# Optimization experiments

Measured on AMD Instinct MI355X. Metric: run time of the kernel, lower is better.

## Reference

```python
import jax, jax.numpy as jnp
import numpy as np

T = 96
CAP_MWH = 800.0
DP_RAMP = 65.0
DT = 0.25
ETA = float(np.sqrt(0.91))
L_MIN = 4
MAX_CHARGE_MWH = 1200.0
P_MAX = 195.0
N = 5 * T  # variable layout: [c, d, yc, yd, soc]
ITERS = 400  # fixed PDHG iterations (stand-in for SCS to eps=1e-5)

_VOFF = {'c': 0, 'd': 1, 'yc': 2, 'yd': 3, 'soc': 4}

def _idx(v, t):
    return _VOFF[v] * T + t

def _build_lp():
    G, h, A, b = [], [], [], []
    def ineq(pairs, rhs):
        r = np.zeros(N)
        for v, t, co in pairs:
            r[_idx(v, t)] += co
        G.append(r); h.append(rhs)
    def eq(pairs, rhs):
        r = np.zeros(N)
        for v, t, co in pairs:
            r[_idx(v, t)] += co
        A.append(r); b.append(rhs)
    for t in range(T):
        ineq([('c', t, 1.0)], P_MAX); ineq([('d', t, 1.0)], P_MAX)
        ineq([('c', t, -1.0)], 0.0); ineq([('d', t, -1.0)], 0.0)
        ineq([('yc', t, -1.0)], 0.0); ineq([('yc', t, 1.0)], 1.0)
        ineq([('yd', t, -1.0)], 0.0); ineq([('yd', t, 1.0)], 1.0)
        ineq([('soc', t, -1.0)], 0.0); ineq([('soc', t, 1.0)], CAP_MWH)
        ineq([('yc', t, 1.0), ('yd', t, 1.0)], 1.0)
        ineq([('c', t, 1.0), ('yc', t, -P_MAX)], 0.0)
        ineq([('d', t, 1.0), ('yd', t, -P_MAX)], 0.0)
    for t in range(1, T):
        ineq([('c', t, 1.0), ('c', t - 1, -1.0)], DP_RAMP)
        ineq([('c', t - 1, 1.0), ('c', t, -1.0)], DP_RAMP)
        ineq([('d', t, 1.0), ('d', t - 1, -1.0)], DP_RAMP)
        ineq([('d', t - 1, 1.0), ('d', t, -1.0)], DP_RAMP)
    for t in range(T - 1):
        ineq([('yc', t, 1.0), ('yd', t + 1, 1.0)], 1.0)
        ineq([('yd', t, 1.0), ('yc', t + 1, 1.0)], 1.0)
    for v in ('yc', 'yd'):
        for t in range(T):
            for k in range(1, L_MIN):
                if t + k >= T:
                    break
                if t > 0:
                    ineq([(v, t + k, -1.0), (v, t, 1.0), (v, t - 1, -1.0)], 0.0)
                else:
                    ineq([(v, t + k, -1.0), (v, t, 1.0)], 0.0)
    ineq([('c', t, DT) for t in range(T)], MAX_CHARGE_MWH)
    eq([('soc', 0, 1.0), ('c', 0, -ETA * DT), ('d', 0, DT / ETA)], 0.0)
    for t in range(1, T):
        eq([('soc', t, 1.0), ('soc', t - 1, -1.0), ('c', t, -ETA * DT), ('d', t, DT / ETA)], 0.0)
    eq([('soc', T - 1, 1.0)], 0.0)
    return np.array(G), np.array(h), np.array(A), np.array(b)

_G, _h, _A, _b = _build_lp()
_M_EQ = _A.shape[0]
_K_np = np.vstack([_A, _G]).astype(np.float32)
_kb_np = np.concatenate([_b, _h]).astype(np.float32)
_LNORM = float(np.linalg.norm(_K_np.astype(np.float64), 2))
TAU = np.float32(0.9 / _LNORM)
SIG = np.float32(0.9 / _LNORM)
K_MAT = jnp.asarray(_K_np)     # (M, N)
KB = jnp.asarray(_kb_np)       # (M,)


def _solve_one(price):
    # LP: min q^T x  s.t.  A x = b, G x <= h   (max price.(d-c)*DT)
    q = DT * jnp.concatenate([price, -price, jnp.zeros(3 * T, price.dtype)])
    def step(carry, _):
        x, y = carry
        x_new = x - TAU * (q + K_MAT.T @ y)
        x_bar = 2.0 * x_new - x
        y_new = y + SIG * (K_MAT @ x_bar - KB)
        # dual cone projection: equality duals free, inequality duals >= 0
        y_new = jnp.concatenate([y_new[:_M_EQ], jnp.maximum(y_new[_M_EQ:], 0.0)])
        return (x_new, y_new), None
    x0 = jnp.zeros(N, price.dtype)
    y0 = jnp.zeros(K_MAT.shape[0], price.dtype)
    (x, _), _ = jax.lax.scan(step, (x0, y0), None, length=ITERS)
    return x[:T], x[T:2 * T]  # (c, d)


def setup_inputs() -> dict:
    key = jax.random.key(0)
    # realistic-ish electricity prices: ~N(400, 100) CNY/MWh
    price = 400.0 + 100.0 * jax.random.normal(key, (256, T), dtype=jnp.float32)
    return {"price_pred": price}


def reference(price_pred):
    c, d = jax.vmap(_solve_one)(price_pred)  # each (B, 96)
    return c, d
```

## Files before the change

### kernel.cpp

```cpp
#include <hip/hip_runtime.h>
#include <math.h>


#define NITER 400
#define PITER 10
#define NY 1874
#define NX 520

__device__ __forceinline__ float wave_sum64(float v) {
  float r = v;
  int x;
  x = __builtin_amdgcn_update_dpp(0, __float_as_int(r), 0x111, 0xf, 0xf, true);
  r += __int_as_float(x);
  x = __builtin_amdgcn_update_dpp(0, __float_as_int(r), 0x112, 0xf, 0xf, true);
  r += __int_as_float(x);
  x = __builtin_amdgcn_update_dpp(0, __float_as_int(r), 0x114, 0xf, 0xf, true);
  r += __int_as_float(x);
  x = __builtin_amdgcn_update_dpp(0, __float_as_int(r), 0x118, 0xf, 0xf, true);
  r += __int_as_float(x);
  x = __builtin_amdgcn_update_dpp(0, __float_as_int(r), 0x142, 0xa, 0xf, true);
  r += __int_as_float(x);
  x = __builtin_amdgcn_update_dpp(0, __float_as_int(r), 0x143, 0xc, 0xf, true);
  r += __int_as_float(x);
  return __int_as_float(__builtin_amdgcn_readlane(__float_as_int(r), 63));
}

__global__ __launch_bounds__(512, 1)
void lp_solve_kernel(const float* __restrict__ price, float* __restrict__ out) {
  __shared__ float sy[NY];
  __shared__ float sxb[NX];
  __shared__ float s_red[8];

  const int tid = threadIdx.x, lane = tid & 63, wid = tid >> 6, bi = blockIdx.x;
  const double ETA_D = sqrt(0.91);
  const float cET = (float)(-(ETA_D * 0.25));
  const float cDE = (float)(0.25 / ETA_D);

  const bool colAct = (tid < 480);
  const int col = colAct ? tid : 479;
  const int vty = col / 96;
  const int t = col - 96 * vty;
  const int wX = 104 * vty + 4 + t;

  const int v01 = vty & 1;
  const int aBC = 1460 + 104 * v01 + t;
  const int aEQ = 1252 + t;
  const int aUM = 1667 + 104 * v01 + t;
  const float ce = v01 ? cDE : cET;
  const float ctc = v01 ? 0.f : 0.25f;

  const int yv = (vty >= 2) ? (vty - 2) : 0;
  const int bv = 624 * yv + t;
  const int bw = 624 * (1 - yv) + t;

  const float ce1 = (t <= 94) ? -1.f : 1.f;
  const int aBS = 1356 + t;

  const int tb = (wid == 0) ? lane : (64 + (lane & 31));
  const bool isBox = (wid == 0) || (wid == 1 && lane < 32);
  int er; bool eqRun, eqAct;
  if (wid == 1)      { er = (lane >= 32) ? lane - 32 : 0; eqRun = true; eqAct = (lane >= 32); }
  else if (wid == 5) { er = 32 + lane; eqRun = true; eqAct = true; }
  else if (wid == 7) { er = 96; eqRun = true; eqAct = (lane == 32); }
  else               { er = 0; eqRun = false; eqAct = false; }
  const float cEb = (er == 96) ? -1.f : 1.f;
  const bool mdRun = (wid >= 2) && (wid <= 4);
  const int mi0 = ((wid - 2) << 6) + lane;
  const bool mdAct = mdRun && (mi0 < 190);
  const int mi = mdAct ? mi0 : 189;
  const int mv = (mi >= 95) ? 1 : 0;
  const int mt = mi - 95 * mv;
  const int mx = 104 * (2 + mv) + mt;
  const int mw = 624 * mv + mt;
  const float cv2 = (mt <= 93) ? 1.f : 0.f;
  const float cv3 = (mt <= 92) ? 1.f : 0.f;
  const bool rRun = (wid == 5) || (wid == 6);
  const bool rAct = (wid == 5) || (wid == 6 && lane < 31);
  const int rt = (wid == 5) ? (1 + lane) : (65 + ((lane < 31) ? lane : 30));
  const bool sRun = (wid >= 6);
  const bool sAct = (wid == 6) || (wid == 7 && lane < 31);
  const int st = (wid == 6) ? lane : (64 + ((lane < 31) ? lane : 30));

  float xA = 0.f, qA = 0.f;
  float yb0=0,yb1=0,yb2=0,yb3=0,yb4=0,yb5=0,yb6=0,yb7=0,yb8=0,yb9=0,yb10=0,yb11=0,yb12=0;
  float ym1=0, ym2=0, ym3=0, yr0=0, yr1=0, yr2=0, yr3=0, ysw0=0, ysw1=0, yeq=0, ytc=0;

  auto gatherA = [&]() -> float {
    if (wid < 3) {
      float b = sy[aBC], e = sy[aEQ];
      float um = sy[aUM], up = sy[aUM + 1];
      float tc = sy[1872];
      return b + ce * e + um - up + ctc * tc;
    } else if (wid < 6) {
      float k1 = sy[bv + 3], k2 = sy[bv + 106], k3 = sy[bv + 209];
      float m0 = sy[bv + 316], m1 = sy[bv + 317];
      float bY = sy[bv + 420], s0 = sy[bv + 524], s1 = sy[bw + 523];
      return bY + s0 + s1 + (m0 - m1) - (k1 + k2 + k3);
    } else {
      float e0 = sy[aEQ], e1 = sy[aEQ + 1], bS = sy[aBS];
      return bS + e0 + ce1 * e1;
    }
  };

  float tauv = 0.f, sigv = 0.f;
  auto phaseBfull = [&](bool power) {
    const float sig = sigv;
    if (wid <= 1) {
      float c_ = sxb[4 + tb], d_ = sxb[108 + tb];
      float yc_ = sxb[212 + tb], yd_ = sxb[316 + tb], s_ = sxb[420 + tb];
      float v0,v1,v2,v3,v4,v5,v6,v7,v8,v9,v10,v11,v12;
      if (power) {
        v0=c_; v1=d_; v2=-c_; v3=-d_; v4=-yc_; v5=yc_; v6=-yd_; v7=yd_;
        v8=-s_; v9=s_; v10=yc_+yd_; v11=c_-195.f*yc_; v12=d_-195.f*yd_;
      } else {
        yb0  = fmaxf(yb0  + sig*(c_  - 195.f), 0.f);      v0 = yb0;
        yb1  = fmaxf(yb1  + sig*(d_  - 195.f), 0.f);      v1 = yb1;
        yb2  = fmaxf(yb2  - sig*c_,            0.f);      v2 = yb2;
        yb3  = fmaxf(yb3  - sig*d_,            0.f);      v3 = yb3;
        yb4  = fmaxf(yb4  - sig*yc_,           0.f);      v4 = yb4;
        yb5  = fmaxf(yb5  + sig*(yc_ - 1.f),   0.f);      v5 = yb5;
        yb6  = fmaxf(yb6  - sig*yd_,           0.f);      v6 = yb6;
        yb7  = fmaxf(yb7  + sig*(yd_ - 1.f),   0.f);      v7 = yb7;
        yb8  = fmaxf(yb8  - sig*s_,            0.f);      v8 = yb8;
        yb9  = fmaxf(yb9  + sig*(s_ - 800.f),  0.f);      v9 = yb9;
        yb10 = fmaxf(yb10 + sig*(yc_ + yd_ - 1.f), 0.f);  v10 = yb10;
        yb11 = fmaxf(yb11 + sig*(c_ - 195.f*yc_), 0.f);   v11 = yb11;
        yb12 = fmaxf(yb12 + sig*(d_ - 195.f*yd_), 0.f);   v12 = yb12;
      }
      if (isBox) {
        sy[1460 + tb] = v0 - v2 + v11;
        sy[1564 + tb] = v1 - v3 + v12;
        sy[420 + tb]  = -v4 + v5 + v10 - 195.f * v11;
        sy[1044 + tb] = -v6 + v7 + v10 - 195.f * v12;
        sy[1356 + tb] = -v8 + v9;
      }
    }
    if (mdRun) {
      float mp = sxb[mx + 3];
      float mc = sxb[mx + 4], m1v = sxb[mx + 5];
      float m2v = sxb[mx + 6], m3v = sxb[mx + 7];
      float base = mc - mp;
      float d1 = base - m1v, d2 = base - m2v, d3 = base - m3v;
      float o1, o2, o3;
      if (power) { o1 = d1; o2 = d2; o3 = d3; }
      else {
        ym1 = fmaxf(ym1 + sig * d1, 0.f); o1 = ym1;
        ym2 = fmaxf(ym2 + sig * d2, 0.f); o2 = ym2;
        ym3 = fmaxf(ym3 + sig * d3, 0.f); o3 = ym3;
      }
      if (mdAct) {
        sy[mw + 4]   = o1;
        sy[mw + 108] = o2;
        sy[mw + 212] = o3;
        sy[mw + 316] = o1 + cv2 * o2 + cv3 * o3;
      }
    }
    if (rRun) {
      float rcm = sxb[3 + rt], rc0 = sxb[4 + rt];
      float rdm = sxb[107 + rt], rd0 = sxb[108 + rt];
      float u0, u1, u2, u3;
      if (power) { u0 = rc0 - rcm; u1 = rcm - rc0; u2 = rd0 - rdm; u3 = rdm - rd0; }
      else {
        yr0 = fmaxf(yr0 + sig * (rc0 - rcm - 65.f), 0.f); u0 = yr0;
        yr1 = fmaxf(yr1 + sig * (rcm - rc0 - 65.f), 0.f); u1 = yr1;
        yr2 = fmaxf(yr2 + sig * (rd0 - rdm - 65.f), 0.f); u2 = yr2;
        yr3 = fmaxf(yr3 + sig * (rdm - rd0 - 65.f), 0.f); u3 = yr3;
      }
      if (rAct) { sy[1667 + rt] = u0 - u1; sy[1771 + rt] = u2 - u3; }
    }
    if (sRun) {
      float a0 = sxb[212 + st], a1 = sxb[213 + st];
      float b0 = sxb[316 + st], b1 = sxb[317 + st];
      float p0, p1;
      if (power) { p0 = a0 + b1; p1 = b0 + a1; }
      else {
        ysw0 = fmaxf(ysw0 + sig * (a0 + b1 - 1.f), 0.f); p0 = ysw0;
        ysw1 = fmaxf(ysw1 + sig * (b0 + a1 - 1.f), 0.f); p1 = ysw1;
      }
      if (sAct) { sy[524 + st] = p0; sy[1148 + st] = p1; }
    }
    if (eqRun) {
      float ep = sxb[419 + er], ecur = sxb[420 + er];
      float exc = sxb[4 + er], exd = sxb[108 + er];
      float dot = ecur - cEb * ep + cET * exc + cDE * exd;
      float ev;
      if (power) ev = dot;
      else { yeq += sig * dot; ev = yeq; }
      if (eqAct) sy[1252 + er] = ev;
    }
    if (wid == 7) {
      float ssum = sxb[4 + lane] + ((lane < 32) ? sxb[68 + lane] : 0.f);
      float tot = wave_sum64(ssum);
      float wv;
      if (power) wv = 0.25f * tot;
      else { ytc = fmaxf(ytc + sig * (0.25f * tot - 1200.f), 0.f); wv = ytc; }
      if (lane == 0) sy[1872] = wv;
    }
  };

  for (int i = tid; i < NY; i += 512) sy[i] = 0.f;
  for (int i = tid; i < NX; i += 512) sxb[i] = 0.f;
  __syncthreads();
  if (colAct) sxb[wX] = 1.f;
  __syncthreads();

  float lam2 = 1.f;
  for (int pit = 0; pit < PITER; ++pit) {
    phaseBfull(true);
    __syncthreads();
    float gA = gatherA();
    if (!colAct) gA = 0.f;
    float part = wave_sum64(gA * gA);
    if (lane == 0) s_red[wid] = part;
    __syncthreads();
    lam2 = sqrtf(s_red[0] + s_red[1] + s_red[2] + s_red[3]
               + s_red[4] + s_red[5] + s_red[6] + s_red[7]);
    float inv = 1.f / lam2;
    if (colAct) sxb[wX] = gA * inv;
    __syncthreads();
  }
  tauv = (float)(0.9 / sqrt((double)lam2));
  sigv = tauv;

  for (int i = tid; i < NY; i += 512) sy[i] = 0.f;
  if (tid < 96)       qA =  0.25f * price[bi * 96 + tid];
  else if (tid < 192) qA = -0.25f * price[bi * 96 + (tid - 96)];
  __syncthreads();

#pragma unroll 1
  for (int it = 0; it < NITER; ++it) {
    float gA = gatherA();
    if (colAct) {
      float xa = xA - tauv * (qA + gA);
      sxb[wX] = 2.f * xa - xA;
      xA = xa;
    }
    __syncthreads();
    phaseBfull(false);
    __syncthreads();
  }

  if (tid < 96)       out[bi * 96 + tid] = xA;
  else if (tid < 192) out[24576 + bi * 96 + (tid - 96)] = xA;
}

extern "C" void kernel_launch(void* const* d_in, const int* in_sizes, int n_in,
                              void* d_out, int out_size, void* d_ws, size_t ws_size,
                              hipStream_t stream) {
  const float* price = (const float*)d_in[0];
  float* outp = (float*)d_out;
  hipLaunchKernelGGL(lp_solve_kernel, dim3(256), dim3(512), 0, stream, price, outp);
}
```

Baseline: 259.5 us.

## Solve each LP in a single wavefront with register state and lane shuffles

The 512-thread block that used shared memory and two block barriers per PDHG iteration is replaced by one 64-lane wavefront per problem. Each lane holds two time steps of every variable and dual in registers, and neighbour couplings are exchanged with shuffles instead of LDS. This removes __syncthreads and shared-memory round trips, but each lane now does far more serial arithmetic, only 256 waves run on the GPU, and register pressure rises.

```diff
diff --git a/kernel.cpp b/kernel.cpp
--- a/kernel.cpp
+++ b/kernel.cpp
@@ -4,8 +4,6 @@
 
 #define NITER 400
 #define PITER 10
-#define NY 1874
-#define NX 520
 
 __device__ __forceinline__ float wave_sum64(float v) {
   float r = v;
@@ -25,223 +23,252 @@
   return __int_as_float(__builtin_amdgcn_readlane(__float_as_int(r), 63));
 }
 
-__global__ __launch_bounds__(512, 1)
+__global__ __launch_bounds__(64, 1)
 void lp_solve_kernel(const float* __restrict__ price, float* __restrict__ out) {
-  __shared__ float sy[NY];
-  __shared__ float sxb[NX];
-  __shared__ float s_red[8];
-
-  const int tid = threadIdx.x, lane = tid & 63, wid = tid >> 6, bi = blockIdx.x;
+  const int lane = threadIdx.x;
+  const int bi = blockIdx.x;
   const double ETA_D = sqrt(0.91);
   const float cET = (float)(-(ETA_D * 0.25));
   const float cDE = (float)(0.25 / ETA_D);
 
-  const bool colAct = (tid < 480);
-  const int col = colAct ? tid : 479;
-  const int vty = col / 96;
-  const int t = col - 96 * vty;
-  const int wX = 104 * vty + 4 + t;
-
-  const int v01 = vty & 1;
-  const int aBC = 1460 + 104 * v01 + t;
-  const int aEQ = 1252 + t;
-  const int aUM = 1667 + 104 * v01 + t;
-  const float ce = v01 ? cDE : cET;
-  const float ctc = v01 ? 0.f : 0.25f;
-
-  const int yv = (vty >= 2) ? (vty - 2) : 0;
-  const int bv = 624 * yv + t;
-  const int bw = 624 * (1 - yv) + t;
-
-  const float ce1 = (t <= 94) ? -1.f : 1.f;
-  const int aBS = 1356 + t;
-
-  const int tb = (wid == 0) ? lane : (64 + (lane & 31));
-  const bool isBox = (wid == 0) || (wid == 1 && lane < 32);
-  int er; bool eqRun, eqAct;
-  if (wid == 1)      { er = (lane >= 32) ? lane - 32 : 0; eqRun = true; eqAct = (lane >= 32); }
-  else if (wid == 5) { er = 32 + lane; eqRun = true; eqAct = true; }
-  else if (wid == 7) { er = 96; eqRun = true; eqAct = (lane == 32); }
-  else               { er = 0; eqRun = false; eqAct = false; }
-  const float cEb = (er == 96) ? -1.f : 1.f;
-  const bool mdRun = (wid >= 2) && (wid <= 4);
-  const int mi0 = ((wid - 2) << 6) + lane;
-  const bool mdAct = mdRun && (mi0 < 190);
-  const int mi = mdAct ? mi0 : 189;
-  const int mv = (mi >= 95) ? 1 : 0;
-  const int mt = mi - 95 * mv;
-  const int mx = 104 * (2 + mv) + mt;
-  const int mw = 624 * mv + mt;
-  const float cv2 = (mt <= 93) ? 1.f : 0.f;
-  const float cv3 = (mt <= 92) ? 1.f : 0.f;
-  const bool rRun = (wid == 5) || (wid == 6);
-  const bool rAct = (wid == 5) || (wid == 6 && lane < 31);
-  const int rt = (wid == 5) ? (1 + lane) : (65 + ((lane < 31) ? lane : 30));
-  const bool sRun = (wid >= 6);
-  const bool sAct = (wid == 6) || (wid == 7 && lane < 31);
-  const int st = (wid == 6) ? lane : (64 + ((lane < 31) ? lane : 30));
-
-  float xA = 0.f, qA = 0.f;
-  float yb0=0,yb1=0,yb2=0,yb3=0,yb4=0,yb5=0,yb6=0,yb7=0,yb8=0,yb9=0,yb10=0,yb11=0,yb12=0;
-  float ym1=0, ym2=0, ym3=0, yr0=0, yr1=0, yr2=0, yr3=0, ysw0=0, ysw1=0, yeq=0, ytc=0;
-
-  auto gatherA = [&]() -> float {
-    if (wid < 3) {
-      float b = sy[aBC], e = sy[aEQ];
-      float um = sy[aUM], up = sy[aUM + 1];
-      float tc = sy[1872];
-      return b + ce * e + um - up + ctc * tc;
-    } else if (wid < 6) {
-      float k1 = sy[bv + 3], k2 = sy[bv + 106], k3 = sy[bv + 209];
-      float m0 = sy[bv + 316], m1 = sy[bv + 317];
-      float bY = sy[bv + 420], s0 = sy[bv + 524], s1 = sy[bw + 523];
-      return bY + s0 + s1 + (m0 - m1) - (k1 + k2 + k3);
-    } else {
-      float e0 = sy[aEQ], e1 = sy[aEQ + 1], bS = sy[aBS];
-      return bS + e0 + ce1 * e1;
-    }
+  const float act = (lane < 48) ? 1.f : 0.f;
+  const float m_r[2]  = { (lane >= 1 && lane < 48) ? 1.f : 0.f, act };
+  const float m_sw[2] = { act, (lane <= 46) ? 1.f : 0.f };
+  const float m_md[3][2] = {
+    { act,                        (lane <= 46) ? 1.f : 0.f },
+    { (lane <= 46) ? 1.f : 0.f,   (lane <= 46) ? 1.f : 0.f },
+    { (lane <= 46) ? 1.f : 0.f,   (lane <= 45) ? 1.f : 0.f }
   };
 
-  float tauv = 0.f, sigv = 0.f;
-  auto phaseBfull = [&](bool power) {
-    const float sig = sigv;
-    if (wid <= 1) {
-      float c_ = sxb[4 + tb], d_ = sxb[108 + tb];
-      float yc_ = sxb[212 + tb], yd_ = sxb[316 + tb], s_ = sxb[420 + tb];
-      float v0,v1,v2,v3,v4,v5,v6,v7,v8,v9,v10,v11,v12;
+  auto shup1z = [&](float x) { float y = __shfl_up(x, 1, 64); return (lane >= 1) ? y : 0.f; };
+  auto shup2z = [&](float x) { float y = __shfl_up(x, 2, 64); return (lane >= 2) ? y : 0.f; };
+  auto shdn1  = [&](float x) { return __shfl_down(x, 1, 64); };
+  auto shdn2  = [&](float x) { return __shfl_down(x, 2, 64); };
+
+  float xc[2] = {0, 0}, xd[2] = {0, 0}, xyc[2] = {0, 0}, xyd[2] = {0, 0}, xs[2] = {0, 0};
+  float xbc[2] = {0, 0}, xbd[2] = {0, 0}, xbyc[2] = {0, 0}, xbyd[2] = {0, 0}, xbs[2] = {0, 0};
+  float qc[2] = {0, 0}, qd[2] = {0, 0};
+  float yb[2][13];
+#pragma unroll
+  for (int p = 0; p < 2; ++p)
+#pragma unroll
+    for (int i = 0; i < 13; ++i) yb[p][i] = 0.f;
+  float ymc[2][3] = {{0, 0, 0}, {0, 0, 0}}, ymd[2][3] = {{0, 0, 0}, {0, 0, 0}};
+  float yr[2][4] = {{0, 0, 0, 0}, {0, 0, 0, 0}};
+  float sw0[2] = {0, 0}, sw1[2] = {0, 0};
+  float yeq[2] = {0, 0};
+  float yeq96 = 0.f, ytc = 0.f;
+  float uc[2] = {0, 0}, ud[2] = {0, 0}, msc[2] = {0, 0}, msd[2] = {0, 0};
+
+  float sigv = 0.f, tauv = 0.f;
+  float sa = 0.f, sr[2] = {0, 0}, ssw[2] = {0, 0};
+  float smd[3][2] = {{0, 0}, {0, 0}, {0, 0}};
+
+  auto phaseB = [&](bool power) {
+    float pxc[2], pxd[2], pxs[2], pxyc[2], pxyd[2];
+    pxc[0]  = shup1z(xbc[1]);  pxc[1]  = xbc[0];
+    pxd[0]  = shup1z(xbd[1]);  pxd[1]  = xbd[0];
+    pxs[0]  = shup1z(xbs[1]);  pxs[1]  = xbs[0];
+    pxyc[0] = shup1z(xbyc[1]); pxyc[1] = xbyc[0];
+    pxyd[0] = shup1z(xbyd[1]); pxyd[1] = xbyd[0];
+    float nyc1[2], nyc2[2], nyc3[2], nyd1[2], nyd2[2], nyd3[2];
+    nyc1[1] = shdn1(xbyc[0]); nyc1[0] = xbyc[1];
+    nyc2[1] = shdn1(xbyc[1]); nyc2[0] = nyc1[1];
+    nyc3[1] = shdn2(xbyc[0]); nyc3[0] = nyc2[1];
+    nyd1[1] = shdn1(xbyd[0]); nyd1[0] = xbyd[1];
+    nyd2[1] = shdn1(xbyd[1]); nyd2[0] = nyd1[1];
+    nyd3[1] = shdn2(xbyd[0]); nyd3[0] = nyd2[1];
+
+#pragma unroll
+    for (int p = 0; p < 2; ++p) {
+      const float c_ = xbc[p], d_ = xbd[p], yc_ = xbyc[p], yd_ = xbyd[p], s_ = xbs[p];
       if (power) {
-        v0=c_; v1=d_; v2=-c_; v3=-d_; v4=-yc_; v5=yc_; v6=-yd_; v7=yd_;
-        v8=-s_; v9=s_; v10=yc_+yd_; v11=c_-195.f*yc_; v12=d_-195.f*yd_;
+        yb[p][0] = c_;   yb[p][1] = d_;
+        yb[p][2] = -c_;  yb[p][3] = -d_;
+        yb[p][4] = -yc_; yb[p][5] = yc_;
+        yb[p][6] = -yd_; yb[p][7] = yd_;
+        yb[p][8] = -s_;  yb[p][9] = s_;
+        yb[p][10] = yc_ + yd_;
+        yb[p][11] = c_ - 195.f * yc_;
+        yb[p][12] = d_ - 195.f * yd_;
       } else {
-        yb0  = fmaxf(yb0  + sig*(c_  - 195.f), 0.f);      v0 = yb0;
-        yb1  = fmaxf(yb1  + sig*(d_  - 195.f), 0.f);      v1 = yb1;
-        yb2  = fmaxf(yb2  - sig*c_,            0.f);      v2 = yb2;
-        yb3  = fmaxf(yb3  - sig*d_,            0.f);      v3 = yb3;
-        yb4  = fmaxf(yb4  - sig*yc_,           0.f);      v4 = yb4;
-        yb5  = fmaxf(yb5  + sig*(yc_ - 1.f),   0.f);      v5 = yb5;
-        yb6  = fmaxf(yb6  - sig*yd_,           0.f);      v6 = yb6;
-        yb7  = fmaxf(yb7  + sig*(yd_ - 1.f),   0.f);      v7 = yb7;
-        yb8  = fmaxf(yb8  - sig*s_,            0.f);      v8 = yb8;
-        yb9  = fmaxf(yb9  + sig*(s_ - 800.f),  0.f);      v9 = yb9;
-        yb10 = fmaxf(yb10 + sig*(yc_ + yd_ - 1.f), 0.f);  v10 = yb10;
-        yb11 = fmaxf(yb11 + sig*(c_ - 195.f*yc_), 0.f);   v11 = yb11;
-        yb12 = fmaxf(yb12 + sig*(d_ - 195.f*yd_), 0.f);   v12 = yb12;
-      }
-      if (isBox) {
-        sy[1460 + tb] = v0 - v2 + v11;
-        sy[1564 + tb] = v1 - v3 + v12;
-        sy[420 + tb]  = -v4 + v5 + v10 - 195.f * v11;
-        sy[1044 + tb] = -v6 + v7 + v10 - 195.f * v12;
-        sy[1356 + tb] = -v8 + v9;
-      }
-    }
-    if (mdRun) {
-      float mp = sxb[mx + 3];
-      float mc = sxb[mx + 4], m1v = sxb[mx + 5];
-      float m2v = sxb[mx + 6], m3v = sxb[mx + 7];
-      float base = mc - mp;
-      float d1 = base - m1v, d2 = base - m2v, d3 = base - m3v;
-      float o1, o2, o3;
-      if (power) { o1 = d1; o2 = d2; o3 = d3; }
-      else {
-        ym1 = fmaxf(ym1 + sig * d1, 0.f); o1 = ym1;
-        ym2 = fmaxf(ym2 + sig * d2, 0.f); o2 = ym2;
-        ym3 = fmaxf(ym3 + sig * d3, 0.f); o3 = ym3;
-      }
-      if (mdAct) {
-        sy[mw + 4]   = o1;
-        sy[mw + 108] = o2;
-        sy[mw + 212] = o3;
-        sy[mw + 316] = o1 + cv2 * o2 + cv3 * o3;
-      }
-    }
-    if (rRun) {
-      float rcm = sxb[3 + rt], rc0 = sxb[4 + rt];
-      float rdm = sxb[107 + rt], rd0 = sxb[108 + rt];
-      float u0, u1, u2, u3;
-      if (power) { u0 = rc0 - rcm; u1 = rcm - rc0; u2 = rd0 - rdm; u3 = rdm - rd0; }
-      else {
-        yr0 = fmaxf(yr0 + sig * (rc0 - rcm - 65.f), 0.f); u0 = yr0;
-        yr1 = fmaxf(yr1 + sig * (rcm - rc0 - 65.f), 0.f); u1 = yr1;
-        yr2 = fmaxf(yr2 + sig * (rd0 - rdm - 65.f), 0.f); u2 = yr2;
-        yr3 = fmaxf(yr3 + sig * (rdm - rd0 - 65.f), 0.f); u3 = yr3;
-      }
-      if (rAct) { sy[1667 + rt] = u0 - u1; sy[1771 + rt] = u2 - u3; }
-    }
-    if (sRun) {
-      float a0 = sxb[212 + st], a1 = sxb[213 + st];
-      float b0 = sxb[316 + st], b1 = sxb[317 + st];
-      float p0, p1;
-      if (power) { p0 = a0 + b1; p1 = b0 + a1; }
-      else {
-        ysw0 = fmaxf(ysw0 + sig * (a0 + b1 - 1.f), 0.f); p0 = ysw0;
-        ysw1 = fmaxf(ysw1 + sig * (b0 + a1 - 1.f), 0.f); p1 = ysw1;
-      }
-      if (sAct) { sy[524 + st] = p0; sy[1148 + st] = p1; }
-    }
-    if (eqRun) {
-      float ep = sxb[419 + er], ecur = sxb[420 + er];
-      float exc = sxb[4 + er], exd = sxb[108 + er];
-      float dot = ecur - cEb * ep + cET * exc + cDE * exd;
-      float ev;
-      if (power) ev = dot;
-      else { yeq += sig * dot; ev = yeq; }
-      if (eqAct) sy[1252 + er] = ev;
-    }
-    if (wid == 7) {
-      float ssum = sxb[4 + lane] + ((lane < 32) ? sxb[68 + lane] : 0.f);
-      float tot = wave_sum64(ssum);
-      float wv;
-      if (power) wv = 0.25f * tot;
-      else { ytc = fmaxf(ytc + sig * (0.25f * tot - 1200.f), 0.f); wv = ytc; }
-      if (lane == 0) sy[1872] = wv;
+        yb[p][0]  = fmaxf(yb[p][0]  + sa * (c_ - 195.f), 0.f);
+        yb[p][1]  = fmaxf(yb[p][1]  + sa * (d_ - 195.f), 0.f);
+        yb[p][2]  = fmaxf(yb[p][2]  - sa * c_,           0.f);
+        yb[p][3]  = fmaxf(yb[p][3]  - sa * d_,           0.f);
+        yb[p][4]  = fmaxf(yb[p][4]  - sa * yc_,          0.f);
+        yb[p][5]  = fmaxf(yb[p][5]  + sa * (yc_ - 1.f),  0.f);
+        yb[p][6]  = fmaxf(yb[p][6]  - sa * yd_,          0.f);
+        yb[p][7]  = fmaxf(yb[p][7]  + sa * (yd_ - 1.f),  0.f);
+        yb[p][8]  = fmaxf(yb[p][8]  - sa * s_,           0.f);
+        yb[p][9]  = fmaxf(yb[p][9]  + sa * (s_ - 800.f), 0.f);
+        yb[p][10] = fmaxf(yb[p][10] + sa * (yc_ + yd_ - 1.f), 0.f);
+        yb[p][11] = fmaxf(yb[p][11] + sa * (c_ - 195.f * yc_), 0.f);
+        yb[p][12] = fmaxf(yb[p][12] + sa * (d_ - 195.f * yd_), 0.f);
+      }
+      {
+        float dc1 = yc_ - pxyc[p] - nyc1[p];
+        float dc2 = yc_ - pxyc[p] - nyc2[p];
+        float dc3 = yc_ - pxyc[p] - nyc3[p];
+        float dd1 = yd_ - pxyd[p] - nyd1[p];
+        float dd2 = yd_ - pxyd[p] - nyd2[p];
+        float dd3 = yd_ - pxyd[p] - nyd3[p];
+        if (power) {
+          ymc[p][0] = m_md[0][p] * dc1; ymc[p][1] = m_md[1][p] * dc2; ymc[p][2] = m_md[2][p] * dc3;
+          ymd[p][0] = m_md[0][p] * dd1; ymd[p][1] = m_md[1][p] * dd2; ymd[p][2] = m_md[2][p] * dd3;
+        } else {
+          ymc[p][0] = fmaxf(ymc[p][0] + smd[0][p] * dc1, 0.f);
+          ymc[p][1] = fmaxf(ymc[p][1] + smd[1][p] * dc2, 0.f);
+          ymc[p][2] = fmaxf(ymc[p][2] + smd[2][p] * dc3, 0.f);
+          ymd[p][0] = fmaxf(ymd[p][0] + smd[0][p] * dd1, 0.f);
+          ymd[p][1] = fmaxf(ymd[p][1] + smd[1][p] * dd2, 0.f);
+          ymd[p][2] = fmaxf(ymd[p][2] + smd[2][p] * dd3, 0.f);
+        }
+      }
+      {
+        float dc = c_ - pxc[p], dd = d_ - pxd[p];
+        if (power) {
+          yr[p][0] = m_r[p] * dc; yr[p][1] = -m_r[p] * dc;
+          yr[p][2] = m_r[p] * dd; yr[p][3] = -m_r[p] * dd;
+        } else {
+          yr[p][0] = fmaxf(yr[p][0] + sr[p] * (dc - 65.f),  0.f);
+          yr[p][1] = fmaxf(yr[p][1] + sr[p] * (-dc - 65.f), 0.f);
+          yr[p][2] = fmaxf(yr[p][2] + sr[p] * (dd - 65.f),  0.f);
+          yr[p][3] = fmaxf(yr[p][3] + sr[p] * (-dd - 65.f), 0.f);
+        }
+      }
+      {
+        float d0 = yc_ + nyd1[p], d1 = yd_ + nyc1[p];
+        if (power) { sw0[p] = m_sw[p] * d0; sw1[p] = m_sw[p] * d1; }
+        else {
+          sw0[p] = fmaxf(sw0[p] + ssw[p] * (d0 - 1.f), 0.f);
+          sw1[p] = fmaxf(sw1[p] + ssw[p] * (d1 - 1.f), 0.f);
+        }
+      }
+      {
+        float de = s_ - pxs[p] + cET * c_ + cDE * d_;
+        if (power) yeq[p] = act * de;
+        else yeq[p] += sa * de;
+      }
+      uc[p] = yr[p][0] - yr[p][1];
+      ud[p] = yr[p][2] - yr[p][3];
+      msc[p] = ymc[p][0] + ymc[p][1] + ymc[p][2];
+      msd[p] = ymd[p][0] + ymd[p][1] + ymd[p][2];
+    }
+    {
+      float s95 = __shfl(xbs[1], 47, 64);
+      if (power) yeq96 = s95; else yeq96 += sigv * s95;
+      float tot = wave_sum64(xbc[0] + xbc[1]);
+      if (power) ytc = 0.25f * tot;
+      else ytc = fmaxf(ytc + sigv * (0.25f * tot - 1200.f), 0.f);
     }
   };
 
-  for (int i = tid; i < NY; i += 512) sy[i] = 0.f;
-  for (int i = tid; i < NX; i += 512) sxb[i] = 0.f;
-  __syncthreads();
-  if (colAct) sxb[wX] = 1.f;
-  __syncthreads();
-
+  float gc[2], gd[2], gyc[2], gyd[2], gs[2];
+  auto gather = [&]() {
+    float ucn[2], udn[2], mscn[2], msdn[2], eqn[2];
+    ucn[0] = uc[1];   ucn[1] = shdn1(uc[0]);
+    udn[0] = ud[1];   udn[1] = shdn1(ud[0]);
+    mscn[0] = msc[1]; mscn[1] = shdn1(msc[0]);
+    msdn[0] = msd[1]; msdn[1] = shdn1(msd[0]);
+    eqn[0] = yeq[1];
+    { float tdn = shdn1(yeq[0]); eqn[1] = (lane == 47) ? -yeq96 : tdn; }
+    float sw1p[2], sw0p[2];
+    sw1p[0] = shup1z(sw1[1]); sw1p[1] = sw1[0];
+    sw0p[0] = shup1z(sw0[1]); sw0p[1] = sw0[0];
+    float pc1[2], pc2[2], pc3[2], pd1[2], pd2[2], pd3[2];
+    pc1[0] = shup1z(ymc[1][0]); pc1[1] = ymc[0][0];
+    pc2[0] = shup1z(ymc[0][1]); pc2[1] = shup1z(ymc[1][1]);
+    pc3[0] = shup2z(ymc[1][2]); pc3[1] = shup1z(ymc[0][2]);
+    pd1[0] = shup1z(ymd[1][0]); pd1[1] = ymd[0][0];
+    pd2[0] = shup1z(ymd[0][1]); pd2[1] = shup1z(ymd[1][1]);
+    pd3[0] = shup2z(ymd[1][2]); pd3[1] = shup1z(ymd[0][2]);
+#pragma unroll
+    for (int p = 0; p < 2; ++p) {
+      gc[p] = (yb[p][0] - yb[p][2] + yb[p][11]) + uc[p] - ucn[p]
+            + 0.25f * ytc + cET * yeq[p];
+      gd[p] = (yb[p][1] - yb[p][3] + yb[p][12]) + ud[p] - udn[p] + cDE * yeq[p];
+      gyc[p] = (-yb[p][4] + yb[p][5] + yb[p][10] - 195.f * yb[p][11])
+             + sw0[p] + sw1p[p] + msc[p] - mscn[p] - pc1[p] - pc2[p] - pc3[p];
+      gyd[p] = (-yb[p][6] + yb[p][7] + yb[p][10] - 195.f * yb[p][12])
+             + sw1[p] + sw0p[p] + msd[p] - msdn[p] - pd1[p] - pd2[p] - pd3[p];
+      gs[p] = (-yb[p][8] + yb[p][9]) + yeq[p] - eqn[p];
+    }
+  };
+
+#pragma unroll
+  for (int p = 0; p < 2; ++p) {
+    xbc[p] = act; xbd[p] = act; xbyc[p] = act; xbyd[p] = act; xbs[p] = act;
+  }
   float lam2 = 1.f;
   for (int pit = 0; pit < PITER; ++pit) {
-    phaseBfull(true);
-    __syncthreads();
-    float gA = gatherA();
-    if (!colAct) gA = 0.f;
-    float part = wave_sum64(gA * gA);
-    if (lane == 0) s_red[wid] = part;
-    __syncthreads();
-    lam2 = sqrtf(s_red[0] + s_red[1] + s_red[2] + s_red[3]
-               + s_red[4] + s_red[5] + s_red[6] + s_red[7]);
-    float inv = 1.f / lam2;
-    if (colAct) sxb[wX] = gA * inv;
-    __syncthreads();
+    phaseB(true);
+    gather();
+    float part = gc[0] * gc[0] + gc[1] * gc[1] + gd[0] * gd[0] + gd[1] * gd[1]
+               + gyc[0] * gyc[0] + gyc[1] * gyc[1] + gyd[0] * gyd[0] + gyd[1] * gyd[1]
+               + gs[0] * gs[0] + gs[1] * gs[1];
+    part *= act;
+    lam2 = sqrtf(wave_sum64(part));
+    float inv = act / lam2;
+#pragma unroll
+    for (int p = 0; p < 2; ++p) {
+      xbc[p] = gc[p] * inv; xbd[p] = gd[p] * inv;
+      xbyc[p] = gyc[p] * inv; xbyd[p] = gyd[p] * inv; xbs[p] = gs[p] * inv;
+    }
   }
   tauv = (float)(0.9 / sqrt((double)lam2));
   sigv = tauv;
-
-  for (int i = tid; i < NY; i += 512) sy[i] = 0.f;
-  if (tid < 96)       qA =  0.25f * price[bi * 96 + tid];
-  else if (tid < 192) qA = -0.25f * price[bi * 96 + (tid - 96)];
-  __syncthreads();
-
+  sa = sigv * act;
+  sr[0] = sigv * m_r[0];  sr[1] = sigv * m_r[1];
+  ssw[0] = sigv * m_sw[0]; ssw[1] = sigv * m_sw[1];
+#pragma unroll
+  for (int k = 0; k < 3; ++k) { smd[k][0] = sigv * m_md[k][0]; smd[k][1] = sigv * m_md[k][1]; }
+
+#pragma unroll
+  for (int p = 0; p < 2; ++p) {
+#pragma unroll
+    for (int i = 0; i < 13; ++i) yb[p][i] = 0.f;
+#pragma unroll
+    for (int k = 0; k < 3; ++k) { ymc[p][k] = 0.f; ymd[p][k] = 0.f; }
+#pragma unroll
+    for (int k = 0; k < 4; ++k) yr[p][k] = 0.f;
+    sw0[p] = 0.f; sw1[p] = 0.f; yeq[p] = 0.f;
+    uc[p] = 0.f; ud[p] = 0.f; msc[p] = 0.f; msd[p] = 0.f;
+    xbc[p] = 0.f; xbd[p] = 0.f; xbyc[p] = 0.f; xbyd[p] = 0.f; xbs[p] = 0.f;
+    xc[p] = 0.f; xd[p] = 0.f; xyc[p] = 0.f; xyd[p] = 0.f; xs[p] = 0.f;
+  }
+  yeq96 = 0.f; ytc = 0.f;
+
+  {
+    const int l2 = (lane < 48) ? lane : 0;
+    float p0 = price[bi * 96 + 2 * l2];
+    float p1 = price[bi * 96 + 2 * l2 + 1];
+    qc[0] = 0.25f * p0;  qc[1] = 0.25f * p1;
+    qd[0] = -0.25f * p0; qd[1] = -0.25f * p1;
+  }
+
+  const float ta = tauv * act;
 #pragma unroll 1
   for (int it = 0; it < NITER; ++it) {
-    float gA = gatherA();
-    if (colAct) {
-      float xa = xA - tauv * (qA + gA);
-      sxb[wX] = 2.f * xa - xA;
-      xA = xa;
-    }
-    __syncthreads();
-    phaseBfull(false);
-    __syncthreads();
-  }
-
-  if (tid < 96)       out[bi * 96 + tid] = xA;
-  else if (tid < 192) out[24576 + bi * 96 + (tid - 96)] = xA;
+    gather();
+#pragma unroll
+    for (int p = 0; p < 2; ++p) {
+      float xa;
+      xa = xc[p]  - ta * (qc[p] + gc[p]);  xbc[p]  = 2.f * xa - xc[p];  xc[p]  = xa;
+      xa = xd[p]  - ta * (qd[p] + gd[p]);  xbd[p]  = 2.f * xa - xd[p];  xd[p]  = xa;
+      xa = xyc[p] - ta * gyc[p];           xbyc[p] = 2.f * xa - xyc[p]; xyc[p] = xa;
+      xa = xyd[p] - ta * gyd[p];           xbyd[p] = 2.f * xa - xyd[p]; xyd[p] = xa;
+      xa = xs[p]  - ta * gs[p];            xbs[p]  = 2.f * xa - xs[p];  xs[p]  = xa;
+    }
+    phaseB(false);
+  }
+
+  if (lane < 48) {
+    out[bi * 96 + 2 * lane]             = xc[0];
+    out[bi * 96 + 2 * lane + 1]         = xc[1];
+    out[24576 + bi * 96 + 2 * lane]     = xd[0];
+    out[24576 + bi * 96 + 2 * lane + 1] = xd[1];
+  }
 }
 
 extern "C" void kernel_launch(void* const* d_in, const int* in_sizes, int n_in,
@@ -249,5 +276,5 @@
                               hipStream_t stream) {
   const float* price = (const float*)d_in[0];
   float* outp = (float*)d_out;
-  hipLaunchKernelGGL(lp_solve_kernel, dim3(256), dim3(512), 0, stream, price, outp);
+  hipLaunchKernelGGL(lp_solve_kernel, dim3(256), dim3(64), 0, stream, price, outp);
 }
```

After: 353.6 us. 1.36x slower.
